# Performance work log

Hardware: AMD Instinct MI355X
Metric: run time of the kernel (lower is better)

## Reference

```python
import jax, jax.numpy as jnp
import numpy as np

BATCH, T, H = 2048, 32, 1024
IN_DIM = 2  # [prev_pred, fd_step]

def setup_inputs() -> dict:
    key = jax.random.key(0)
    ks = jax.random.split(key, 9)
    s_ih = 1.0 / np.sqrt(H)
    return {
        "future_fd": jax.random.normal(ks[0], (BATCH, T), jnp.float32),
        "hidden": jax.random.normal(ks[1], (1, BATCH, H), jnp.float32),
        "cell": jax.random.normal(ks[2], (1, BATCH, H), jnp.float32),
        "W_ih": jax.random.uniform(ks[3], (4 * H, IN_DIM), jnp.float32, -s_ih, s_ih),
        "W_hh": jax.random.uniform(ks[4], (4 * H, H), jnp.float32, -s_ih, s_ih),
        "b_ih": jax.random.uniform(ks[5], (4 * H,), jnp.float32, -s_ih, s_ih),
        "b_hh": jax.random.uniform(ks[6], (4 * H,), jnp.float32, -s_ih, s_ih),
        "fc_W": jax.random.uniform(ks[7], (1, H), jnp.float32, -s_ih, s_ih),
        "fc_b": jax.random.uniform(ks[8], (1,), jnp.float32, -s_ih, s_ih),
        "output_len": T,
    }

def reference(future_fd, hidden, cell, W_ih, W_hh, b_ih, b_hh, fc_W, fc_b, output_len):
    # Inference path (targets=None): decoder input is previous prediction.
    h0, c0 = hidden[0], cell[0]            # (B, H), num_layers == 1
    b = b_ih + b_hh                        # (4H,)
    prev0 = jnp.zeros((future_fd.shape[0], 1), future_fd.dtype)

    def step(carry, fd_t):
        h, c, prev = carry
        x = jnp.concatenate([prev, fd_t[:, None]], axis=1)   # (B, 2)
        gates = x @ W_ih.T + h @ W_hh.T + b                  # (B, 4H)
        i, f, g, o = jnp.split(gates, 4, axis=1)             # PyTorch gate order i,f,g,o
        c_new = jax.nn.sigmoid(f) * c + jax.nn.sigmoid(i) * jnp.tanh(g)
        h_new = jax.nn.sigmoid(o) * jnp.tanh(c_new)
        pred = h_new @ fc_W.T + fc_b                          # (B, 1)
        return (h_new, c_new, pred), pred

    _, preds = jax.lax.scan(step, (h0, c0, prev0), future_fd.T)  # (T, B, 1)
    return jnp.transpose(preds, (1, 0, 2))                       # (B, T, 1)
```

## Files before the change

### kernel.cpp

```cpp
#include <hip/hip_runtime.h>
#include <hip/hip_bf16.h>

#define TSTEPS 32
#define HDIM 1024

typedef __bf16 bf16x8 __attribute__((ext_vector_type(8)));
typedef float f32x4 __attribute__((ext_vector_type(4)));
typedef unsigned short u16;
typedef unsigned int u32;

__device__ __forceinline__ u32 f2bf(float f) {
    u32 u = __float_as_uint(f);
    return (u + 0x7FFFu + ((u >> 16) & 1u)) >> 16;
}
__device__ __forceinline__ u32 pack2(float a, float b) {
    return f2bf(a) | (f2bf(b) << 16);
}
__device__ __forceinline__ float bf2f(u16 v) {
    return __uint_as_float(((u32)v) << 16);
}
__device__ __forceinline__ float sigf(float x) { return 1.f / (1.f + __expf(-x)); }
__device__ __forceinline__ float tanhfast(float x) { return 1.f - 2.f / (1.f + __expf(2.f * x)); }

__device__ __forceinline__ void sbar()    { __builtin_amdgcn_s_barrier(); }
__device__ __forceinline__ void vmcnt12() { asm volatile("s_waitcnt vmcnt(12)" ::: "memory"); }
__device__ __forceinline__ void vmcnt8()  { asm volatile("s_waitcnt vmcnt(8)"  ::: "memory"); }
__device__ __forceinline__ void vmcnt0()  { asm volatile("s_waitcnt vmcnt(0)"  ::: "memory"); }
__device__ __forceinline__ void lgkm0()   { asm volatile("s_waitcnt lgkmcnt(0)" ::: "memory"); }


__global__ void k_prep_w(const float* __restrict__ W, const float* __restrict__ Wih,
                         const float* __restrict__ fcW, uint4* __restrict__ Wp) {
    int o = blockIdx.x * 256 + threadIdx.x;
    int colT = o >> 14, c = (o >> 10) & 15, l = o & 1023;
    int bc = l >> 3, u = l & 7;
    int jg = ((bc >> 5) << 10) + colT * 32 + (bc & 31);
    int kk = c * 64 + ((u ^ (bc & 7)) << 3);
    const float4* src  = (const float4*)(W + (size_t)jg * HDIM + kk);
    const float4* fsrc = (const float4*)(fcW + kk);
    float wx = Wih[2 * jg];
    float4 lo = src[0], hi = src[1], fl = fsrc[0], fh = fsrc[1];
    lo.x += wx * fl.x; lo.y += wx * fl.y; lo.z += wx * fl.z; lo.w += wx * fl.w;
    hi.x += wx * fh.x; hi.y += wx * fh.y; hi.z += wx * fh.z; hi.w += wx * fh.w;
    uint4 pk = { pack2(lo.x, lo.y), pack2(lo.z, lo.w), pack2(hi.x, hi.y), pack2(hi.z, hi.w) };
    Wp[o] = pk;
}

__global__ void k_prep_state(const float* __restrict__ h0, const float* __restrict__ c0,
                             u16* __restrict__ hb, u16* __restrict__ c) {
    int i = blockIdx.x * 256 + threadIdx.x;
    float4 v = ((const float4*)h0)[i];
    float4 cv = ((const float4*)c0)[i];
    ushort4 o  = { (u16)f2bf(v.x),  (u16)f2bf(v.y),  (u16)f2bf(v.z),  (u16)f2bf(v.w) };
    ushort4 oc = { (u16)f2bf(cv.x), (u16)f2bf(cv.y), (u16)f2bf(cv.z), (u16)f2bf(cv.w) };
    ((ushort4*)hb)[i] = o;
    ((ushort4*)c)[i] = oc;
}

__global__ void k_prep_p0(const float* __restrict__ h0, const float* __restrict__ fcW,
                          const float* __restrict__ fcb, float* __restrict__ p0) {
    int n = blockIdx.x * 4 + (threadIdx.x >> 6);
    int lane = threadIdx.x & 63;
    const float* hr = h0 + (size_t)n * HDIM;
    float s = 0.f;
#pragma unroll
    for (int i = 0; i < 16; ++i)
        s += fcW[lane + 64 * i] * hr[lane + 64 * i];
    s += __shfl_xor(s, 1);  s += __shfl_xor(s, 2);  s += __shfl_xor(s, 4);
    s += __shfl_xor(s, 8);  s += __shfl_xor(s, 16); s += __shfl_xor(s, 32);
    if (lane == 0) p0[n] = s + fcb[0];
}

__global__ void k_init_out(float* __restrict__ out, const float* __restrict__ fcb) {
    int i = blockIdx.x * 256 + threadIdx.x;
    out[i] = fcb[0];
}

__device__ __forceinline__ void stage_chunk(const uint4* __restrict__ g, uint4* dst, int tid) {
    const uint4* g0 = g + tid;
    uint4* l0 = dst + (tid & ~63);
#pragma unroll
    for (int i = 0; i < 4; ++i)
        __builtin_amdgcn_global_load_lds(
            (const __attribute__((address_space(1))) void*)(g0 + i * 512),
            (__attribute__((address_space(3))) void*)(l0 + i * 512), 16, 0, 0);
}

__global__ __launch_bounds__(512, 4) void k_step(
    const u16* __restrict__ hin, u16* __restrict__ hout,
    u16* __restrict__ c, const uint4* __restrict__ Wp,
    const float* __restrict__ fd, const float* __restrict__ Wih,
    const float* __restrict__ bih, const float* __restrict__ bhh,
    const float* __restrict__ fcw, const float* __restrict__ fcb,
    const float* __restrict__ p0, float* out, int t)
{
    __shared__ uint4 lbuf[2][2048];
    __shared__ float pp[2][128];

    const int tid  = threadIdx.x;
    const int lane = tid & 63;
    const int wave = tid >> 6;
    const int lr = lane & 15, lk = lane >> 4;
    const int wc = wave & 1, wr = wave >> 1;
    const int id  = blockIdx.x;
    const int xcd = id & 7, kk = id >> 3;
    const int colT = ((xcd & 3) << 3) + (kk & 7);
    const int rowT = ((xcd >> 2) << 3) + (kk >> 3);
    const uint4* wbase = Wp + colT * 16384;

    const u16* arow = hin + (size_t)(rowT * 128 + wr * 32 + lr) * HDIM + lk * 8;

    f32x4 acc[2][4];
#pragma unroll
    for (int a = 0; a < 2; ++a)
#pragma unroll
        for (int g = 0; g < 4; ++g)
            acc[a][g] = (f32x4){0.f, 0.f, 0.f, 0.f};

    bf16x8 A0[2][4], A1[2][4];

    stage_chunk(wbase, &lbuf[0][0], tid);
#pragma unroll
    for (int kcl = 0; kcl < 4; ++kcl) {
        A0[0][kcl] = *(const bf16x8*)(arow + kcl * 32);
        A1[0][kcl] = *(const bf16x8*)(arow + 16 * HDIM + kcl * 32);
    }
    vmcnt8();
    sbar();

#pragma unroll
    for (int ch = 0; ch < 8; ++ch) {
        if (ch < 7) {
            stage_chunk(wbase + (ch + 1) * 2048, &lbuf[(ch + 1) & 1][0], tid);
#pragma unroll
            for (int kcl = 0; kcl < 4; ++kcl) {
                const int kg = (ch + 1) * 4 + kcl;
                A0[(ch + 1) & 1][kcl] = *(const bf16x8*)(arow + kg * 32);
                A1[(ch + 1) & 1][kcl] = *(const bf16x8*)(arow + 16 * HDIM + kg * 32);
            }
            vmcnt12();
        } else {
            vmcnt0();
        }
        if (ch > 0) sbar();

        const uint4* buf = &lbuf[ch & 1][0];
#pragma unroll
        for (int kcl = 0; kcl < 4; ++kcl) {
            bf16x8 a0 = A0[ch & 1][kcl];
            bf16x8 a1 = A1[ch & 1][kcl];
#pragma unroll
            for (int cf = 0; cf < 4; ++cf) {
                const int bc = cf * 32 + wc * 16 + lr;
                uint4 braw = buf[(kcl >> 1) * 1024 + bc * 8 +
                                 ((((kcl & 1) << 2) + lk) ^ (bc & 7))];
                bf16x8 bfr = __builtin_bit_cast(bf16x8, braw);
                acc[0][cf] = __builtin_amdgcn_mfma_f32_16x16x32_bf16(a0, bfr, acc[0][cf], 0, 0, 0);
                acc[1][cf] = __builtin_amdgcn_mfma_f32_16x16x32_bf16(a1, bfr, acc[1][cf], 0, 0, 0);
            }
        }
        if (ch < 7) {
            lgkm0();
            sbar();
        }
    }

    const int j = colT * 32 + wc * 16 + lr;
    float wx0[4], wx1[4], bs[4];
#pragma unroll
    for (int g = 0; g < 4; ++g) {
        int gr = g * HDIM + j;
        wx0[g] = Wih[2 * gr];
        wx1[g] = Wih[2 * gr + 1];
        bs[g]  = bih[gr] + bhh[gr];
    }
    const float fcwj = fcw[j];
    const float fcbv = fcb[0];

#pragma unroll
    for (int ar = 0; ar < 2; ++ar)
#pragma unroll
        for (int r = 0; r < 4; ++r) {
            const int n = rowT * 128 + wr * 32 + ar * 16 + lk * 4 + r;
            float fdv  = fd[n * TSTEPS + t];
            float pc   = (t == 0) ? (fcbv - p0[n]) : fcbv;
            float gi = acc[ar][0][r] + wx1[0] * fdv + bs[0] + wx0[0] * pc;
            float gf = acc[ar][1][r] + wx1[1] * fdv + bs[1] + wx0[1] * pc;
            float gg = acc[ar][2][r] + wx1[2] * fdv + bs[2] + wx0[2] * pc;
            float go = acc[ar][3][r] + wx1[3] * fdv + bs[3] + wx0[3] * pc;
            float cold = bf2f(c[(size_t)n * HDIM + j]);
            float cn = sigf(gf) * cold + sigf(gi) * tanhfast(gg);
            c[(size_t)n * HDIM + j] = (u16)f2bf(cn);
            float hn = sigf(go) * tanhfast(cn);
            hout[(size_t)n * HDIM + j] = (u16)f2bf(hn);
            float pr = fcwj * hn;
            pr += __shfl_xor(pr, 1);
            pr += __shfl_xor(pr, 2);
            pr += __shfl_xor(pr, 4);
            pr += __shfl_xor(pr, 8);
            if (lr == 0) pp[wc][wr * 32 + ar * 16 + lk * 4 + r] = pr;
        }
    __syncthreads();
    if (tid < 128) {
        int n = rowT * 128 + tid;
        atomicAdd(&out[n * TSTEPS + t], pp[0][tid] + pp[1][tid]);
    }
}

extern "C" void kernel_launch(void* const* d_in, const int* in_sizes, int n_in,
                              void* d_out, int out_size, void* d_ws, size_t ws_size,
                              hipStream_t stream) {
    const float* fd  = (const float*)d_in[0];
    const float* h0  = (const float*)d_in[1];
    const float* c0  = (const float*)d_in[2];
    const float* Wih = (const float*)d_in[3];
    const float* Whh = (const float*)d_in[4];
    const float* bih = (const float*)d_in[5];
    const float* bhh = (const float*)d_in[6];
    const float* fcw = (const float*)d_in[7];
    const float* fcb = (const float*)d_in[8];
    float* out = (float*)d_out;

    char* ws = (char*)d_ws;
    uint4* Wp   = (uint4*)(ws);
    u16*   hb0  = (u16*)(ws + 8388608);
    u16*   hb1  = (u16*)(ws + 12582912);
    u16*   cbuf = (u16*)(ws + 16777216);
    float* p0   = (float*)(ws + 25165824);

    k_prep_w    <<<dim3(2048), dim3(256), 0, stream>>>(Whh, Wih, fcw, Wp);
    k_prep_state<<<dim3(2048), dim3(256), 0, stream>>>(h0, c0, hb0, cbuf);
    k_prep_p0   <<<dim3(512),  dim3(256), 0, stream>>>(h0, fcw, fcb, p0);
    k_init_out  <<<dim3(256),  dim3(256), 0, stream>>>(out, fcb);

    for (int t = 0; t < TSTEPS; ++t) {
        const u16* hi = (t & 1) ? hb1 : hb0;
        u16*       ho = (t & 1) ? hb0 : hb1;
        k_step<<<dim3(512), dim3(512), 0, stream>>>(hi, ho, cbuf, Wp, fd,
                                                     Wih, bih, bhh, fcw, fcb,
                                                     p0, out, t);
    }
}
```

Before: 1.387 ms.

## Replace per-timestep launches with a cooperative persistent kernel using row-group barriers

Fuses the 32 per-step kernel launches and the state/output init into one cooperative persistent kernel with 256 blocks of 1024 threads. Blocks sync through atomic-counter barriers scoped to the 16 blocks that share a row tile, instead of kernel boundaries. The cell state now lives in fp32 registers rather than a bf16 global buffer, and each block covers two column tiles. This removes launch overhead and repeated state loads, at the cost of spin-wait barriers and a dependence on co-residency. If the cooperative launch fails, the code falls back to the old multi-launch path.

```diff
diff --git a/kernel.cpp b/kernel.cpp
--- a/kernel.cpp
+++ b/kernel.cpp
@@ -46,6 +46,22 @@
     Wp[o] = pk;
 }
 
+__global__ void k_prep_p0(const float* __restrict__ h0, const float* __restrict__ fcW,
+                          const float* __restrict__ fcb, float* __restrict__ p0) {
+    int n = blockIdx.x * 4 + (threadIdx.x >> 6);
+    int lane = threadIdx.x & 63;
+    const float* hr = h0 + (size_t)n * HDIM;
+    float s = 0.f;
+#pragma unroll
+    for (int i = 0; i < 16; ++i)
+        s += fcW[lane + 64 * i] * hr[lane + 64 * i];
+    s += __shfl_xor(s, 1);  s += __shfl_xor(s, 2);  s += __shfl_xor(s, 4);
+    s += __shfl_xor(s, 8);  s += __shfl_xor(s, 16); s += __shfl_xor(s, 32);
+    if (lane == 0) p0[n] = s + fcb[0];
+}
+
+__global__ void k_zero(u32* __restrict__ cnt) { cnt[threadIdx.x] = 0; }
+
 __global__ void k_prep_state(const float* __restrict__ h0, const float* __restrict__ c0,
                              u16* __restrict__ hb, u16* __restrict__ c) {
     int i = blockIdx.x * 256 + threadIdx.x;
@@ -57,23 +73,188 @@
     ((ushort4*)c)[i] = oc;
 }
 
-__global__ void k_prep_p0(const float* __restrict__ h0, const float* __restrict__ fcW,
-                          const float* __restrict__ fcb, float* __restrict__ p0) {
-    int n = blockIdx.x * 4 + (threadIdx.x >> 6);
-    int lane = threadIdx.x & 63;
-    const float* hr = h0 + (size_t)n * HDIM;
-    float s = 0.f;
-#pragma unroll
-    for (int i = 0; i < 16; ++i)
-        s += fcW[lane + 64 * i] * hr[lane + 64 * i];
-    s += __shfl_xor(s, 1);  s += __shfl_xor(s, 2);  s += __shfl_xor(s, 4);
-    s += __shfl_xor(s, 8);  s += __shfl_xor(s, 16); s += __shfl_xor(s, 32);
-    if (lane == 0) p0[n] = s + fcb[0];
-}
-
 __global__ void k_init_out(float* __restrict__ out, const float* __restrict__ fcb) {
     int i = blockIdx.x * 256 + threadIdx.x;
     out[i] = fcb[0];
+}
+
+
+__device__ __forceinline__ void stage2(const uint4* __restrict__ w0,
+                                       const uint4* __restrict__ w1,
+                                       uint4* dst, int tid) {
+    const int hf = tid >> 9;
+    const int tl = tid & 511;
+    const uint4* src = (hf ? w1 : w0) + tl;
+    uint4* l0 = dst + hf * 2048 + (tl & ~63);
+#pragma unroll
+    for (int i = 0; i < 4; ++i)
+        __builtin_amdgcn_global_load_lds(
+            (const __attribute__((address_space(1))) void*)(src + i * 512),
+            (__attribute__((address_space(3))) void*)(l0 + i * 512), 16, 0, 0);
+}
+
+__device__ __forceinline__ void xbar(u32* cnt, u32 target, int tid) {
+    __syncthreads();
+    if (tid == 0) {
+        __builtin_amdgcn_fence(__ATOMIC_RELEASE, "agent");
+        __hip_atomic_fetch_add(cnt, 1u, __ATOMIC_RELEASE, __HIP_MEMORY_SCOPE_AGENT);
+        while (__hip_atomic_load(cnt, __ATOMIC_RELAXED, __HIP_MEMORY_SCOPE_AGENT) < target)
+            __builtin_amdgcn_s_sleep(2);
+    }
+    __syncthreads();
+    __builtin_amdgcn_fence(__ATOMIC_ACQUIRE, "agent");
+}
+
+__global__ __launch_bounds__(1024, 4) void k_persist(
+    const float* __restrict__ fd, const float* __restrict__ h0,
+    const float* __restrict__ c0, const float* __restrict__ Wih,
+    const float* __restrict__ bih, const float* __restrict__ bhh,
+    const float* __restrict__ fcw, const float* __restrict__ fcb,
+    const float* __restrict__ p0, const uint4* __restrict__ Wp,
+    u16* hb0, u16* hb1, u32* cntbase, float* out)
+{
+    __shared__ uint4 lbuf[2][4096];
+    __shared__ float pp[4][128];
+
+    const int tid  = threadIdx.x;
+    const int lane = tid & 63;
+    const int wave = tid >> 6;
+    const int lr = lane & 15, lk = lane >> 4;
+    const int wc = wave & 3, wr = wave >> 2;
+    const int wcL = wc & 1, hfw = wc >> 1;
+    const int id   = blockIdx.x;
+    const int rowT = id & 15, colP = id >> 4;
+    const int rowbase = rowT * 128;
+    const uint4* wbase0 = Wp + (size_t)(colP * 2) * 16384;
+    const uint4* wbase1 = wbase0 + 16384;
+    u32* cnt = cntbase + rowT * 64;
+
+    {
+        int row = rowbase + (tid >> 3);
+        int j0  = colP * 64 + (tid & 7) * 8;
+        const float* hp = h0 + (size_t)row * HDIM + j0;
+        float4 lo = *(const float4*)hp, hi = *(const float4*)(hp + 4);
+        uint4 pk = { pack2(lo.x, lo.y), pack2(lo.z, lo.w),
+                     pack2(hi.x, hi.y), pack2(hi.z, hi.w) };
+        *(uint4*)(hb0 + (size_t)row * HDIM + j0) = pk;
+    }
+    const float fcbv = fcb[0];
+    if (colP == 0) {
+        int n = rowbase + (tid >> 3);
+        int t0 = (tid & 7) * 4;
+        float4 v = { fcbv, fcbv, fcbv, fcbv };
+        *(float4*)(out + n * TSTEPS + t0) = v;
+    }
+    const int j = colP * 64 + hfw * 32 + wcL * 16 + lr;
+    float creg[2][4];
+#pragma unroll
+    for (int ar = 0; ar < 2; ++ar)
+#pragma unroll
+        for (int r = 0; r < 4; ++r)
+            creg[ar][r] = c0[(size_t)(rowbase + wr * 32 + ar * 16 + lk * 4 + r) * HDIM + j];
+    float wx0[4], wx1[4], bs[4];
+#pragma unroll
+    for (int g = 0; g < 4; ++g) {
+        int gr = g * HDIM + j;
+        wx0[g] = Wih[2 * gr];
+        wx1[g] = Wih[2 * gr + 1];
+        bs[g]  = bih[gr] + bhh[gr];
+    }
+    const float fcwj = fcw[j];
+
+    xbar(cnt, 16, tid);
+
+#pragma unroll 1
+    for (int t = 0; t < TSTEPS; ++t) {
+        const u16* hin = (t & 1) ? hb1 : hb0;
+        u16*      hout = (t & 1) ? hb0 : hb1;
+        const u16* arow = hin + (size_t)(rowbase + wr * 32 + lr) * HDIM + lk * 8;
+
+        f32x4 acc[2][4];
+#pragma unroll
+        for (int a = 0; a < 2; ++a)
+#pragma unroll
+            for (int g = 0; g < 4; ++g)
+                acc[a][g] = (f32x4){0.f, 0.f, 0.f, 0.f};
+
+        bf16x8 A0[2][4], A1[2][4];
+        stage2(wbase0, wbase1, &lbuf[0][0], tid);
+#pragma unroll
+        for (int kcl = 0; kcl < 4; ++kcl) {
+            A0[0][kcl] = *(const bf16x8*)(arow + kcl * 32);
+            A1[0][kcl] = *(const bf16x8*)(arow + 16 * HDIM + kcl * 32);
+        }
+        vmcnt8();
+        sbar();
+
+#pragma unroll
+        for (int ch = 0; ch < 8; ++ch) {
+            if (ch < 7) {
+                stage2(wbase0 + (ch + 1) * 2048, wbase1 + (ch + 1) * 2048,
+                       &lbuf[(ch + 1) & 1][0], tid);
+#pragma unroll
+                for (int kcl = 0; kcl < 4; ++kcl) {
+                    const int kg = (ch + 1) * 4 + kcl;
+                    A0[(ch + 1) & 1][kcl] = *(const bf16x8*)(arow + kg * 32);
+                    A1[(ch + 1) & 1][kcl] = *(const bf16x8*)(arow + 16 * HDIM + kg * 32);
+                }
+                vmcnt12();
+            } else {
+                vmcnt0();
+            }
+            if (ch > 0) sbar();
+
+            const uint4* buf = &lbuf[ch & 1][0];
+#pragma unroll
+            for (int kcl = 0; kcl < 4; ++kcl) {
+                bf16x8 a0 = A0[ch & 1][kcl];
+                bf16x8 a1 = A1[ch & 1][kcl];
+#pragma unroll
+                for (int cf = 0; cf < 4; ++cf) {
+                    const int bcL = cf * 32 + wcL * 16 + lr;
+                    uint4 braw = buf[hfw * 2048 + (kcl >> 1) * 1024 + bcL * 8 +
+                                     ((((kcl & 1) << 2) + lk) ^ (bcL & 7))];
+                    bf16x8 bfr = __builtin_bit_cast(bf16x8, braw);
+                    acc[0][cf] = __builtin_amdgcn_mfma_f32_16x16x32_bf16(a0, bfr, acc[0][cf], 0, 0, 0);
+                    acc[1][cf] = __builtin_amdgcn_mfma_f32_16x16x32_bf16(a1, bfr, acc[1][cf], 0, 0, 0);
+                }
+            }
+            if (ch < 7) {
+                lgkm0();
+                sbar();
+            }
+        }
+
+#pragma unroll
+        for (int ar = 0; ar < 2; ++ar)
+#pragma unroll
+            for (int r = 0; r < 4; ++r) {
+                const int n = rowbase + wr * 32 + ar * 16 + lk * 4 + r;
+                float fdv = fd[n * TSTEPS + t];
+                float pc  = (t == 0) ? (fcbv - p0[n]) : fcbv;
+                float gi = acc[ar][0][r] + wx1[0] * fdv + bs[0] + wx0[0] * pc;
+                float gf = acc[ar][1][r] + wx1[1] * fdv + bs[1] + wx0[1] * pc;
+                float gg = acc[ar][2][r] + wx1[2] * fdv + bs[2] + wx0[2] * pc;
+                float go = acc[ar][3][r] + wx1[3] * fdv + bs[3] + wx0[3] * pc;
+                float cn = sigf(gf) * creg[ar][r] + sigf(gi) * tanhfast(gg);
+                creg[ar][r] = cn;
+                float hn = sigf(go) * tanhfast(cn);
+                hout[(size_t)n * HDIM + j] = (u16)f2bf(hn);
+                float pr = fcwj * hn;
+                pr += __shfl_xor(pr, 1);
+                pr += __shfl_xor(pr, 2);
+                pr += __shfl_xor(pr, 4);
+                pr += __shfl_xor(pr, 8);
+                if (lr == 0) pp[wc][wr * 32 + ar * 16 + lk * 4 + r] = pr;
+            }
+        __syncthreads();
+        if (tid < 128) {
+            int n = rowbase + tid;
+            atomicAdd(&out[n * TSTEPS + t], pp[0][tid] + pp[1][tid] + pp[2][tid] + pp[3][tid]);
+        }
+
+        if (t < TSTEPS - 1) xbar(cnt, 16u * (t + 2), tid);
+    }
 }
 
 __device__ __forceinline__ void stage_chunk(const uint4* __restrict__ g, uint4* dst, int tid) {
@@ -118,7 +299,6 @@
             acc[a][g] = (f32x4){0.f, 0.f, 0.f, 0.f};
 
     bf16x8 A0[2][4], A1[2][4];
-
     stage_chunk(wbase, &lbuf[0][0], tid);
 #pragma unroll
     for (int kcl = 0; kcl < 4; ++kcl) {
@@ -225,19 +405,30 @@
     uint4* Wp   = (uint4*)(ws);
     u16*   hb0  = (u16*)(ws + 8388608);
     u16*   hb1  = (u16*)(ws + 12582912);
-    u16*   cbuf = (u16*)(ws + 16777216);
-    float* p0   = (float*)(ws + 25165824);
-
-    k_prep_w    <<<dim3(2048), dim3(256), 0, stream>>>(Whh, Wih, fcw, Wp);
-    k_prep_state<<<dim3(2048), dim3(256), 0, stream>>>(h0, c0, hb0, cbuf);
-    k_prep_p0   <<<dim3(512),  dim3(256), 0, stream>>>(h0, fcw, fcb, p0);
-    k_init_out  <<<dim3(256),  dim3(256), 0, stream>>>(out, fcb);
-
-    for (int t = 0; t < TSTEPS; ++t) {
-        const u16* hi = (t & 1) ? hb1 : hb0;
-        u16*       ho = (t & 1) ? hb0 : hb1;
-        k_step<<<dim3(512), dim3(512), 0, stream>>>(hi, ho, cbuf, Wp, fd,
-                                                     Wih, bih, bhh, fcw, fcb,
-                                                     p0, out, t);
-    }
-}
+    u32*   cnt  = (u32*)(ws + 16777216);
+    float* p0   = (float*)(ws + 16781312);
+    u16*   cbuf = (u16*)(ws + 20971520);
+
+    k_prep_w <<<dim3(2048), dim3(256), 0, stream>>>(Whh, Wih, fcw, Wp);
+    k_prep_p0<<<dim3(512),  dim3(256), 0, stream>>>(h0, fcw, fcb, p0);
+    k_zero   <<<dim3(1),    dim3(1024), 0, stream>>>(cnt);
+
+    void* kargs[] = { (void*)&fd, (void*)&h0, (void*)&c0, (void*)&Wih,
+                      (void*)&bih, (void*)&bhh, (void*)&fcw, (void*)&fcb,
+                      (void*)&p0, (void*)&Wp, (void*)&hb0, (void*)&hb1,
+                      (void*)&cnt, (void*)&out };
+    hipError_t err = hipLaunchCooperativeKernel((const void*)k_persist,
+                                                dim3(256), dim3(1024),
+                                                kargs, 0, stream);
+    if (err != hipSuccess) {
+        k_prep_state<<<dim3(2048), dim3(256), 0, stream>>>(h0, c0, hb0, cbuf);
+        k_init_out  <<<dim3(256),  dim3(256), 0, stream>>>(out, fcb);
+        for (int t = 0; t < TSTEPS; ++t) {
+            const u16* hi = (t & 1) ? hb1 : hb0;
+            u16*       ho = (t & 1) ? hb0 : hb1;
+            k_step<<<dim3(512), dim3(512), 0, stream>>>(hi, ho, cbuf, Wp, fd,
+                                                         Wih, bih, bhh, fcw, fcb,
+                                                         p0, out, t);
+        }
+    }
+}
```

Measured after the change: 3.042 ms. 119% more time.
